# Optimization experiments

Measured on AMD Instinct MI355X. Metric: run time of the kernel, lower is better.

## Reference

```python
import jax, jax.numpy as jnp
import numpy as np

EPS = 1e-8       # module eps
LN_EPS = 1e-5    # torch LayerNorm default
TEMP = 1.0       # relevance_temperature
STRENGTH = 1.0   # reweight_strength default (None -> 1.0)

Q, W, A = 64, 16, 64
D, C, H = 512, 512, 512


def _ln(x, g, b):
    m = x.mean(-1, keepdims=True)
    v = ((x - m) ** 2).mean(-1, keepdims=True)
    return (x - m) / jnp.sqrt(v + LN_EPS) * g + b


def _mlp(x, g, b, w1, b1, w2, b2):
    # LayerNorm -> Linear -> GELU(exact) -> Linear
    h = jax.nn.gelu(_ln(x, g, b) @ w1 + b1, approximate=False)
    return h @ w2 + b2


def setup_inputs() -> dict:
    key = jax.random.key(0)
    ks = iter(jax.random.split(key, 40))
    s = 0.02

    def lin(din, dout):
        return (jax.random.normal(next(ks), (din, dout), jnp.float32) * s,
                jnp.zeros((dout,), jnp.float32))

    inp = {
        "query_atoms": jax.random.normal(next(ks), (Q, A, D), jnp.float32),
        "query_masses": jax.random.uniform(next(ks), (Q, A), jnp.float32, 0.01, 1.0),
        "class_atoms": jax.random.normal(next(ks), (W, A, D), jnp.float32),
        "class_masses": jax.random.uniform(next(ks), (W, A), jnp.float32, 0.01, 1.0),
        "class_summary": jax.random.normal(next(ks), (W, C), jnp.float32),
        "episode_context": jax.random.normal(next(ks), (W, C), jnp.float32),
    }
    # query_proj
    inp["qg"], inp["qb"] = jnp.ones((D,), jnp.float32), jnp.zeros((D,), jnp.float32)
    inp["qw1"], inp["qb1"] = lin(D, H)
    inp["qw2"], inp["qb2"] = lin(H, H)
    # atom_proj
    inp["ag"], inp["ab"] = jnp.ones((D,), jnp.float32), jnp.zeros((D,), jnp.float32)
    inp["aw1"], inp["ab1"] = lin(D, H)
    inp["aw2"], inp["ab2"] = lin(H, H)
    # context_proj (input 2*C)
    inp["cg"], inp["cb"] = jnp.ones((2 * C,), jnp.float32), jnp.zeros((2 * C,), jnp.float32)
    inp["cw1"], inp["cb1"] = lin(2 * C, H)
    inp["cw2"], inp["cb2"] = lin(H, H)
    # relevance_head (input 4*H, output 1)
    inp["rg"], inp["rb"] = jnp.ones((4 * H,), jnp.float32), jnp.zeros((4 * H,), jnp.float32)
    inp["rw1"], inp["rb1"] = lin(4 * H, H)
    inp["rw2"], inp["rb2"] = lin(H, 1)
    return inp


def reference(query_atoms, query_masses, class_atoms, class_masses,
              class_summary, episode_context,
              qg, qb, qw1, qb1, qw2, qb2,
              ag, ab, aw1, ab1, aw2, ab2,
              cg, cb, cw1, cb1, cw2, cb2,
              rg, rb, rw1, rb1, rw2, rb2):
    # normalize query masses, pool query atoms -> [Q, D]
    qm = jnp.maximum(query_masses, 0.0)
    qm = qm / jnp.maximum(qm.sum(-1, keepdims=True), EPS)
    pooled = jnp.einsum('qa,qad->qd', qm, query_atoms)

    qh = _mlp(pooled, qg, qb, qw1, qb1, qw2, qb2)            # [Q, H]
    ah = _mlp(class_atoms, ag, ab, aw1, ab1, aw2, ab2)       # [W, A, H]
    ch = _mlp(jnp.concatenate([class_summary, episode_context], -1),
              cg, cb, cw1, cb1, cw2, cb2)                    # [W, H]

    nq, (way, na, h) = qh.shape[0], ah.shape
    a4 = jnp.broadcast_to(ah[None], (nq, way, na, h))
    q4 = jnp.broadcast_to(qh[:, None, None, :], (nq, way, na, h))
    c4 = jnp.broadcast_to(ch[None, :, None, :], (nq, way, na, h))
    fused = jnp.concatenate([a4, q4, a4 * q4, jnp.abs(a4 - q4) + c4], -1)  # [Q,W,A,4H]

    relevance = _mlp(fused, rg, rb, rw1, rb1, rw2, rb2)[..., 0]  # [Q, W, A]

    combined = jnp.log(jnp.maximum(class_masses, EPS))[None] + relevance / TEMP
    rew = jax.nn.softmax(combined, axis=-1)
    mixed = (1.0 - STRENGTH) * class_masses[None] + STRENGTH * rew
    mixed = mixed / jnp.maximum(mixed.sum(-1, keepdims=True), EPS)
    entropy = -(mixed * jnp.log(jnp.maximum(mixed, EPS))).sum(-1)  # [Q, W]
    return mixed, entropy
```

## Files before the change

kernel.cpp:

```cpp
#include <hip/hip_runtime.h>


#define DEV static __device__ __forceinline__

typedef __attribute__((ext_vector_type(8))) __bf16 bf16x8;
typedef __attribute__((ext_vector_type(4))) float f32x4;
typedef unsigned short ushort_t;

DEV ushort_t f2bf(float f) {
  unsigned u = __builtin_bit_cast(unsigned, f);
  u = (u + 0x7fffu + ((u >> 16) & 1u)) >> 16;
  return (ushort_t)u;
}

DEV float gelu_fast(float x) {
  const float y = x * 0.70710678118654752f;
  const float z = fabsf(y);
  const float t = __fdividef(1.0f, 1.0f + 0.3275911f * z);
  float p = 1.061405429f;
  p = p * t - 1.453152027f;
  p = p * t + 1.421413741f;
  p = p * t - 0.284496736f;
  p = p * t + 0.254829592f;
  const float e = 1.0f - p * t * __expf(-z * z);
  const float erfv = copysignf(e, y);
  return 0.5f * x * (1.0f + erfv);
}

DEV float gelu_sig(float x) {
  return x * __frcp_rn(1.0f + __expf(-1.702f * x));
}

#define OFF_XQB    0
#define OFF_XAB    16384
#define OFF_XCB    278528
#define OFF_HAB    286720
#define OFF_HQB    548864
#define OFF_HCB    565248
#define OFF_AHB    569344
#define OFF_QH     1093632
#define OFF_S1     1126400
#define OFF_B1     1126912
#define OFF_WT2    1127424
#define OFF_RW1LOT 1389568
#define OFF_RW1MIT 1520640
#define OFF_AW1T   1651712
#define OFF_QW1T   1782784
#define OFF_CW1T   1913856
#define OFF_AW2T   2176000
#define OFF_QW2T   2307072
#define OFF_CW2T   2438144
#define OFF_YA     OFF_AW1T
#define OFF_YQ     OFF_AW2T
#define OFF_CHH    OFF_XCB
#define OFF_AHHS   OFF_XAB
#define OFF_QHS    OFF_XQB


DEV void transpose_tile(const float* __restrict__ src, int koff, int kt, int ct,
                        ushort_t* __restrict__ dst, int ldk, float* sh, int tid) {
  float (*t)[65] = (float(*)[65])sh;
  for (int idx = tid; idx < 4096; idx += 512) {
    const int r = idx >> 6, c = idx & 63;
    t[r][c] = src[(koff + kt + r) * 512 + ct + c];
  }
  __syncthreads();
  for (int idx = tid; idx < 4096; idx += 512) {
    const int c = idx >> 6, r = idx & 63;
    dst[(ct + c) * ldk + kt + r] = f2bf(t[r][c]);
  }
}

__global__ __launch_bounds__(512) void pre0_kernel(
    const float* __restrict__ qa, const float* __restrict__ qm,
    const float* __restrict__ ca, const float* __restrict__ csum,
    const float* __restrict__ ectx,
    const float* __restrict__ qg, const float* __restrict__ qb,
    const float* __restrict__ ag, const float* __restrict__ ab,
    const float* __restrict__ cg, const float* __restrict__ cb,
    const float* __restrict__ rw1, const float* __restrict__ rg,
    const float* __restrict__ rb,
    const float* __restrict__ aw1, const float* __restrict__ qw1,
    const float* __restrict__ cw1, const float* __restrict__ aw2,
    const float* __restrict__ qw2, const float* __restrict__ cw2,
    float* __restrict__ ws) {
  __shared__ float sh[4160];
  const int b = blockIdx.x, tid = threadIdx.x, l = tid & 63, wv = tid >> 6;

  if (b < 128) {
    ushort_t* WT = (ushort_t*)(ws + OFF_WT2);
    float (*t)[65] = (float(*)[65])sh;
    const int kt = (b >> 3) << 6;
    const int ct = (b & 7) << 6;
    for (int idx = tid; idx < 4096; idx += 512) {
      const int r = idx >> 6, c = idx & 63;
      t[r][c] = rg[1024 + kt + r] * rw1[(1024 + kt + r) * 512 + ct + c];
    }
    __syncthreads();
    for (int idx = tid; idx < 4096; idx += 512) {
      const int c = idx >> 6, r = idx & 63;
      const int n = ct + c, k2 = kt + r;
      WT[((k2 >> 5) << 14) + (n << 5) + (k2 & 31)] = f2bf(t[r][c]);
    }
  } else if (b < 192) {
    const int bb = b - 128;
    transpose_tile(rw1, 0, (bb >> 3) << 6, (bb & 7) << 6,
                   (ushort_t*)(ws + OFF_RW1LOT), 512, sh, tid);
  } else if (b < 256) {
    const int bb = b - 192;
    transpose_tile(rw1, 512, (bb >> 3) << 6, (bb & 7) << 6,
                   (ushort_t*)(ws + OFF_RW1MIT), 512, sh, tid);
  } else if (b < 320) {
    const int bb = b - 256;
    transpose_tile(aw1, 0, (bb >> 3) << 6, (bb & 7) << 6,
                   (ushort_t*)(ws + OFF_AW1T), 512, sh, tid);
  } else if (b < 384) {
    const int bb = b - 320;
    transpose_tile(qw1, 0, (bb >> 3) << 6, (bb & 7) << 6,
                   (ushort_t*)(ws + OFF_QW1T), 512, sh, tid);
  } else if (b < 512) {
    const int bb = b - 384;
    transpose_tile(cw1, 0, (bb >> 3) << 6, (bb & 7) << 6,
                   (ushort_t*)(ws + OFF_CW1T), 1024, sh, tid);
  } else if (b < 576) {
    const int bb = b - 512;
    transpose_tile(aw2, 0, (bb >> 3) << 6, (bb & 7) << 6,
                   (ushort_t*)(ws + OFF_AW2T), 512, sh, tid);
  } else if (b < 640) {
    const int bb = b - 576;
    transpose_tile(qw2, 0, (bb >> 3) << 6, (bb & 7) << 6,
                   (ushort_t*)(ws + OFF_QW2T), 512, sh, tid);
  } else if (b < 704) {
    const int bb = b - 640;
    transpose_tile(cw2, 0, (bb >> 3) << 6, (bb & 7) << 6,
                   (ushort_t*)(ws + OFF_CW2T), 512, sh, tid);
  } else if (b < 720) {
    const int kc = (b - 704) << 7;
    float s0 = 0.f, s1 = 0.f, b0 = 0.f, b1v = 0.f;
    for (int k = kc; k < kc + 128; k += 2) {
      const float wa = rw1[(k << 9) + tid];
      const float wb = rw1[((k + 1) << 9) + tid];
      s0 += rg[k] * wa; b0 += rb[k] * wa;
      s1 += rg[k + 1] * wb; b1v += rb[k + 1] * wb;
    }
    atomicAdd(ws + OFF_S1 + tid, s0 + s1);
    atomicAdd(ws + OFF_B1 + tid, b0 + b1v);
  } else if (b < 784) {
    const int q = b - 720;
    if (wv == 0) {
      float m = fmaxf(qm[(q << 6) + l], 0.f);
      sh[l] = m;
      float s = m;
#pragma unroll
      for (int off = 1; off < 64; off <<= 1) s += __shfl_xor(s, off);
      if (l == 0) sh[64] = 1.0f / fmaxf(s, 1e-8f);
    }
    __syncthreads();
    const float sinv = sh[64];
    const float* qaq = qa + (q << 15) + tid;
    float v0 = 0.f, v1 = 0.f, v2 = 0.f, v3 = 0.f;
#pragma unroll 4
    for (int a = 0; a < 64; a += 4) {
      v0 += sh[a] * qaq[a << 9];
      v1 += sh[a + 1] * qaq[(a + 1) << 9];
      v2 += sh[a + 2] * qaq[(a + 2) << 9];
      v3 += sh[a + 3] * qaq[(a + 3) << 9];
    }
    const float v = (v0 + v1 + v2 + v3) * sinv;
    float s = v, ss = v * v;
#pragma unroll
    for (int off = 1; off < 64; off <<= 1) {
      s += __shfl_xor(s, off); ss += __shfl_xor(ss, off);
    }
    if (l == 0) { sh[128 + wv] = s; sh[136 + wv] = ss; }
    __syncthreads();
    float st = 0.f, sst = 0.f;
#pragma unroll
    for (int i = 0; i < 8; ++i) { st += sh[128 + i]; sst += sh[136 + i]; }
    const float mu = st * (1.0f / 512.0f);
    const float rstd = rsqrtf(sst * (1.0f / 512.0f) - mu * mu + 1e-5f);
    ((ushort_t*)(ws + OFF_XQB))[(q << 9) + tid] =
        f2bf((v - mu) * rstd * qg[tid] + qb[tid]);
  } else if (b < 912) {
    const int row = ((b - 784) << 3) + wv;
    const float* crow = ca + (row << 9);
    float x[8];
    float s = 0.f, ss = 0.f;
#pragma unroll
    for (int i = 0; i < 8; ++i) {
      x[i] = crow[l + (i << 6)];
      s += x[i]; ss += x[i] * x[i];
    }
#pragma unroll
    for (int off = 1; off < 64; off <<= 1) {
      s += __shfl_xor(s, off); ss += __shfl_xor(ss, off);
    }
    const float mu = s * (1.0f / 512.0f);
    const float rstd = rsqrtf(ss * (1.0f / 512.0f) - mu * mu + 1e-5f);
    ushort_t* xab = (ushort_t*)(ws + OFF_XAB);
#pragma unroll
    for (int i = 0; i < 8; ++i) {
      const int k = l + (i << 6);
      xab[(row << 9) + k] = f2bf((x[i] - mu) * rstd * ag[k] + ab[k]);
    }
  } else {
    const int w = b - 912;
    const float v0 = csum[(w << 9) + tid];
    const float v1 = ectx[(w << 9) + tid];
    float s = v0 + v1, ss = v0 * v0 + v1 * v1;
#pragma unroll
    for (int off = 1; off < 64; off <<= 1) {
      s += __shfl_xor(s, off); ss += __shfl_xor(ss, off);
    }
    if (l == 0) { sh[wv] = s; sh[8 + wv] = ss; }
    __syncthreads();
    float st = 0.f, sst = 0.f;
#pragma unroll
    for (int i = 0; i < 8; ++i) { st += sh[i]; sst += sh[8 + i]; }
    const float mu = st * (1.0f / 1024.0f);
    const float rstd = rsqrtf(sst * (1.0f / 1024.0f) - mu * mu + 1e-5f);
    ushort_t* xcb = (ushort_t*)(ws + OFF_XCB);
    xcb[(w << 10) + tid] = f2bf((v0 - mu) * rstd * cg[tid] + cb[tid]);
    xcb[(w << 10) + 512 + tid] =
        f2bf((v1 - mu) * rstd * cg[512 + tid] + cb[512 + tid]);
  }
}

template <int PHASE>
__global__ __launch_bounds__(256) void gemm_kernel(
    float* __restrict__ ws, const float* __restrict__ ba,
    const float* __restrict__ bq, const float* __restrict__ bc,
    const float* __restrict__ rg) {
  const int b = blockIdx.x, tid = threadIdx.x;
  const int l = tid & 63, wv = tid >> 6;

  const ushort_t* A; const ushort_t* BT;
  float* outF = nullptr; ushort_t* outB = nullptr; ushort_t* outS = nullptr;
  ushort_t* outU = nullptr;
  const float* bias = nullptr; const float* scl = nullptr;
  int K, t;

  if (PHASE == 1) {
    if (b < 512) {
      A = (const ushort_t*)(ws + OFF_XAB); BT = (const ushort_t*)(ws + OFF_AW1T);
      K = 512; outB = (ushort_t*)(ws + OFF_HAB); bias = ba;
      t = (b << 2) + wv;
    } else if (b < 544) {
      A = (const ushort_t*)(ws + OFF_XQB); BT = (const ushort_t*)(ws + OFF_QW1T);
      K = 512; outB = (ushort_t*)(ws + OFF_HQB); bias = bq;
      t = ((b - 512) << 2) + wv;
    } else {
      A = (const ushort_t*)(ws + OFF_XCB); BT = (const ushort_t*)(ws + OFF_CW1T);
      K = 1024; outB = (ushort_t*)(ws + OFF_HCB); bias = bc;
      t = ((b - 544) << 2) + wv;
    }
  } else if (PHASE == 2) {
    if (b < 512) {
      A = (const ushort_t*)(ws + OFF_HAB); BT = (const ushort_t*)(ws + OFF_AW2T);
      K = 512; outU = (ushort_t*)(ws + OFF_AHB);
      outS = (ushort_t*)(ws + OFF_AHHS); bias = ba; scl = rg;
      t = (b << 2) + wv;
    } else if (b < 544) {
      A = (const ushort_t*)(ws + OFF_HQB); BT = (const ushort_t*)(ws + OFF_QW2T);
      K = 512; outF = ws + OFF_QH;
      outS = (ushort_t*)(ws + OFF_QHS); bias = bq; scl = rg + 512;
      t = ((b - 512) << 2) + wv;
    } else {
      A = (const ushort_t*)(ws + OFF_HCB); BT = (const ushort_t*)(ws + OFF_CW2T);
      K = 512; outF = ws + OFF_CHH; bias = bc;
      t = ((b - 544) << 2) + wv;
    }
  } else {
    if (b < 512) {
      A = (const ushort_t*)(ws + OFF_AHHS); BT = (const ushort_t*)(ws + OFF_RW1LOT);
      K = 512; outF = ws + OFF_YA;
      t = (b << 2) + wv;
    } else {
      A = (const ushort_t*)(ws + OFF_QHS); BT = (const ushort_t*)(ws + OFF_RW1MIT);
      K = 512; outF = ws + OFF_YQ;
      t = ((b - 512) << 2) + wv;
    }
  }

  const int rt = t >> 5, ct = t & 31;
  const int r0 = rt << 4, c0 = ct << 4;
  const int kh = (l >> 4) << 3;
  const ushort_t* ap = A + (r0 + (l & 15)) * K + kh;
  const ushort_t* bp = BT + (c0 + (l & 15)) * K + kh;

  f32x4 acc = {};
  const int nst = K >> 5;
#pragma unroll 8
  for (int ks = 0; ks < nst; ++ks) {
    const bf16x8 afr = __builtin_bit_cast(bf16x8, *(const uint4*)(ap + (ks << 5)));
    const bf16x8 bfr = __builtin_bit_cast(bf16x8, *(const uint4*)(bp + (ks << 5)));
    acc = __builtin_amdgcn_mfma_f32_16x16x32_bf16(afr, bfr, acc, 0, 0, 0);
  }

  const int rsub = (l >> 4) << 2, col = c0 + (l & 15);
#pragma unroll
  for (int j = 0; j < 4; ++j) {
    const int row = r0 + rsub + j;
    float v = acc[j];
    if (PHASE == 1) {
      outB[(row << 9) + col] = f2bf(gelu_fast(v + bias[col]));
    } else if (PHASE == 2) {
      v += bias[col];
      if (outU) outU[(row << 9) + col] = f2bf(v);
      if (outF) outF[(row << 9) + col] = v;
      if (outS) outS[(row << 9) + col] = f2bf(v * scl[col]);
    } else {
      outF[(row << 9) + col] = v;
    }
  }
}

__global__ __launch_bounds__(512, 2) void main_kernel(
    const ushort_t* __restrict__ AHB, const float* __restrict__ QH,
    const float* __restrict__ CH, const ushort_t* __restrict__ WT2,
    const float* __restrict__ Ya, const float* __restrict__ Yq,
    const float* __restrict__ S1, const float* __restrict__ B1,
    const float* __restrict__ rb1, const float* __restrict__ rw2,
    const float* __restrict__ rb2, const float* __restrict__ cmass,
    float* __restrict__ out) {
  extern __shared__ char smem_raw[];
  float* qs = (float*)smem_raw;
  float* cs = qs + 1024;
  float* s1_s = cs + 512;
  float* s2_s = s1_s + 128;
  float* rel_s = s2_s + 128;
  float* misc = rel_s + 128;
  uint4* ab4 = (uint4*)(smem_raw + 8192);
  uint4* apv = (uint4*)(smem_raw + 8192 + 65536);

  const int tid = threadIdx.x;
  const int l = tid & 63;
  const int wv = tid >> 6;
  const int w = blockIdx.x & 15;
  const int q0 = (blockIdx.x >> 4) << 1;

  {
    const uint4* src = (const uint4*)(AHB + ((w << 6) << 9));
#pragma unroll
    for (int i = 0; i < 16; ++i) {
      const int u = tid + (i << 9);
      const int row = u >> 7, c16 = u & 127;
      ab4[(row << 7) + (c16 ^ (row & 7))] = src[u];
    }
  }
  qs[tid] = QH[(q0 << 9) + tid];
  qs[tid + 512] = QH[(q0 << 9) + 512 + tid];
  cs[tid] = CH[(w << 9) + tid];
  if (tid < 128) { s1_s[tid] = 0.f; s2_s[tid] = 0.f; rel_s[tid] = 0.f; }
  __syncthreads();

  const int p = wv >> 2;
  const int s = wv & 3;
  const int rloc = (s << 4) + (l & 15);
  const float* qsrc = qs + (p << 9);
  const int kh = (l >> 4) << 3;
  const int ar_base = rloc << 7;
  const int rsw = rloc & 7;
  float s1a = 0.f, s2a = 0.f;

#define BUILD(C, B) do { \
    _Pragma("unroll") for (int ksl_ = 0; ksl_ < 4; ++ksl_) { \
      const int kg_ = ((C) << 7) + (ksl_ << 5) + kh; \
      const int ka_ = kg_ & 511; \
      const bf16x8 av8_ = __builtin_bit_cast(bf16x8, \
          ab4[ar_base + ((ka_ >> 3) ^ rsw)]); \
      union { __bf16 bv[8]; uint4 u4; } pk_; \
      _Pragma("unroll") for (int h_ = 0; h_ < 2; ++h_) { \
        const float4 qv_ = *(const float4*)(qsrc + ka_ + (h_ << 2)); \
        const float a0_ = (float)av8_[(h_ << 2) + 0]; \
        const float a1_ = (float)av8_[(h_ << 2) + 1]; \
        const float a2_ = (float)av8_[(h_ << 2) + 2]; \
        const float a3_ = (float)av8_[(h_ << 2) + 3]; \
        float v0_, v1_, v2_, v3_; \
        if ((C) < 4) { \
          v0_ = a0_ * qv_.x; v1_ = a1_ * qv_.y; \
          v2_ = a2_ * qv_.z; v3_ = a3_ * qv_.w; \
          s1a += (a0_ + a1_ + a2_ + a3_) + (v0_ + v1_ + v2_ + v3_); \
          s2a += (a0_ * a0_ + a1_ * a1_ + a2_ * a2_ + a3_ * a3_) + \
                 (v0_ * v0_ + v1_ * v1_ + v2_ * v2_ + v3_ * v3_); \
        } else { \
          const float4 c_ = *(const float4*)(cs + ka_ + (h_ << 2)); \
          v0_ = fabsf(a0_ - qv_.x) + c_.x; \
          v1_ = fabsf(a1_ - qv_.y) + c_.y; \
          v2_ = fabsf(a2_ - qv_.z) + c_.z; \
          v3_ = fabsf(a3_ - qv_.w) + c_.w; \
          s1a += v0_ + v1_ + v2_ + v3_; \
          s2a += v0_ * v0_ + v1_ * v1_ + v2_ * v2_ + v3_ * v3_; \
        } \
        pk_.bv[(h_ << 2) + 0] = (__bf16)v0_; \
        pk_.bv[(h_ << 2) + 1] = (__bf16)v1_; \
        pk_.bv[(h_ << 2) + 2] = (__bf16)v2_; \
        pk_.bv[(h_ << 2) + 3] = (__bf16)v3_; \
      } \
      apv[((B) << 11) + (p << 10) + (ksl_ << 8) + (s << 6) + l] = pk_.u4; \
    } } while (0)

  BUILD(0, 0);
  if ((wv & 3) == 0) {
    float sq = 0.f, sqq = 0.f;
#pragma unroll
    for (int it = 0; it < 8; ++it) {
      const float vq = qsrc[l + (it << 6)];
      sq += vq; sqq += vq * vq;
    }
#pragma unroll
    for (int off = 1; off < 64; off <<= 1) {
      sq += __shfl_xor(sq, off); sqq += __shfl_xor(sqq, off);
    }
    if (l == 0) { misc[(p << 1)] = sq; misc[(p << 1) + 1] = sqq; }
  }
  __syncthreads();

  f32x4 acc0[4][4] = {}, acc1[4][4] = {};
  const int ncb = (wv << 6) + (l & 15);
  const int boff = (ncb << 5) + kh;
#pragma unroll
  for (int c = 0; c < 8; ++c) {
    if (c < 7) {
      BUILD(c + 1, (c + 1) & 1);
    } else {
      s1a += __shfl_xor(s1a, 16); s1a += __shfl_xor(s1a, 32);
      s2a += __shfl_xor(s2a, 16); s2a += __shfl_xor(s2a, 32);
      if ((l >> 4) == 0) {
        atomicAdd(&s1_s[(p << 6) + rloc], s1a);
        atomicAdd(&s2_s[(p << 6) + rloc], s2a);
      }
    }
    const uint4* cbuf = apv + ((c & 1) << 11);
    const ushort_t* wb = WT2 + ((c << 2) << 14) + boff;
    uint4 bn0 = *(const uint4*)(wb);
    uint4 bn1 = *(const uint4*)(wb + (16 << 5));
    uint4 bn2 = *(const uint4*)(wb + (32 << 5));
    uint4 bn3 = *(const uint4*)(wb + (48 << 5));
#pragma unroll
    for (int ksl = 0; ksl < 4; ++ksl) {
      const bf16x8 bf0 = __builtin_bit_cast(bf16x8, bn0);
      const bf16x8 bf1 = __builtin_bit_cast(bf16x8, bn1);
      const bf16x8 bf2 = __builtin_bit_cast(bf16x8, bn2);
      const bf16x8 bf3 = __builtin_bit_cast(bf16x8, bn3);
      if (ksl < 3) {
        const ushort_t* wn = wb + ((ksl + 1) << 14);
        bn0 = *(const uint4*)(wn);
        bn1 = *(const uint4*)(wn + (16 << 5));
        bn2 = *(const uint4*)(wn + (32 << 5));
        bn3 = *(const uint4*)(wn + (48 << 5));
      }
      bf16x8 afr;
      __builtin_amdgcn_s_setprio(1);
#pragma unroll
      for (int fr = 0; fr < 4; ++fr) {
        afr = __builtin_bit_cast(bf16x8, cbuf[(ksl << 8) + (fr << 6) + l]);
        acc0[fr][0] = __builtin_amdgcn_mfma_f32_16x16x32_bf16(afr, bf0, acc0[fr][0], 0, 0, 0);
        acc0[fr][1] = __builtin_amdgcn_mfma_f32_16x16x32_bf16(afr, bf1, acc0[fr][1], 0, 0, 0);
        acc0[fr][2] = __builtin_amdgcn_mfma_f32_16x16x32_bf16(afr, bf2, acc0[fr][2], 0, 0, 0);
        acc0[fr][3] = __builtin_amdgcn_mfma_f32_16x16x32_bf16(afr, bf3, acc0[fr][3], 0, 0, 0);
      }
#pragma unroll
      for (int fr = 0; fr < 4; ++fr) {
        afr = __builtin_bit_cast(bf16x8, cbuf[(1 << 10) + (ksl << 8) + (fr << 6) + l]);
        acc1[fr][0] = __builtin_amdgcn_mfma_f32_16x16x32_bf16(afr, bf0, acc1[fr][0], 0, 0, 0);
        acc1[fr][1] = __builtin_amdgcn_mfma_f32_16x16x32_bf16(afr, bf1, acc1[fr][1], 0, 0, 0);
        acc1[fr][2] = __builtin_amdgcn_mfma_f32_16x16x32_bf16(afr, bf2, acc1[fr][2], 0, 0, 0);
        acc1[fr][3] = __builtin_amdgcn_mfma_f32_16x16x32_bf16(afr, bf3, acc1[fr][3], 0, 0, 0);
      }
      __builtin_amdgcn_s_setprio(0);
    }
    __syncthreads();
  }
#undef BUILD

  if (tid < 128) {
    const int pp = tid >> 6;
    const float s1r = s1_s[tid] + misc[pp << 1];
    const float s2r = s2_s[tid] + misc[(pp << 1) + 1];
    const float mu = s1r * (1.0f / 2048.0f);
    const float rs = rsqrtf(s2r * (1.0f / 2048.0f) - mu * mu + 1e-5f);
    s1_s[tid] = mu;
    s2_s[tid] = rs;
  }
  __syncthreads();

  {
    float yqv0[4], yqv1[4], s1c[4], b1c[4], w2c[4];
#pragma unroll
    for (int cf = 0; cf < 4; ++cf) {
      const int n = ncb + (cf << 4);
      yqv0[cf] = Yq[(q0 << 9) + n];
      yqv1[cf] = Yq[((q0 + 1) << 9) + n];
      s1c[cf] = S1[n];
      b1c[cf] = B1[n] + rb1[n];
      w2c[cf] = rw2[n];
    }
    const float* yab = Ya + (w << 15) + ncb;
    const int rsub = (l >> 4) << 2;
#pragma unroll
    for (int fr = 0; fr < 4; ++fr) {
#pragma unroll
      for (int j = 0; j < 4; ++j) {
        const int r = (fr << 4) + rsub + j;
        const float mu0 = s1_s[r], rs0 = s2_s[r];
        const float mu1 = s1_s[64 + r], rs1 = s2_s[64 + r];
        float rp0 = 0.f, rp1 = 0.f;
#pragma unroll
        for (int cf = 0; cf < 4; ++cf) {
          const float ya = yab[(r << 9) + (cf << 4)];
          const float c0v = ya + yqv0[cf] - mu0 * s1c[cf];
          const float c1v = ya + yqv1[cf] - mu1 * s1c[cf];
          rp0 += gelu_sig(fmaf(rs0, acc0[fr][cf][j] + c0v, b1c[cf])) * w2c[cf];
          rp1 += gelu_sig(fmaf(rs1, acc1[fr][cf][j] + c1v, b1c[cf])) * w2c[cf];
        }
        rp0 += __shfl_xor(rp0, 1); rp0 += __shfl_xor(rp0, 2);
        rp0 += __shfl_xor(rp0, 4); rp0 += __shfl_xor(rp0, 8);
        rp1 += __shfl_xor(rp1, 1); rp1 += __shfl_xor(rp1, 2);
        rp1 += __shfl_xor(rp1, 4); rp1 += __shfl_xor(rp1, 8);
        if ((l & 15) == 0) {
          atomicAdd(&rel_s[r], rp0);
          atomicAdd(&rel_s[64 + r], rp1);
        }
      }
    }
  }
  __syncthreads();

  if (tid < 128) {
    const int pp = tid >> 6, a = tid & 63;
    const int qw = ((q0 + pp) << 4) + w;
    const float relv = rel_s[(pp << 6) + a] + rb2[0];
    const float x = logf(fmaxf(cmass[(w << 6) + a], 1e-8f)) + relv;
    float m = x;
#pragma unroll
    for (int off = 1; off < 64; off <<= 1) m = fmaxf(m, __shfl_xor(m, off));
    const float pv = expf(x - m);
    float sv = pv;
#pragma unroll
    for (int off = 1; off < 64; off <<= 1) sv += __shfl_xor(sv, off);
    float mix = pv / fmaxf(sv, 1e-8f);
    float s2 = mix;
#pragma unroll
    for (int off = 1; off < 64; off <<= 1) s2 += __shfl_xor(s2, off);
    mix = mix / fmaxf(s2, 1e-8f);
    const float et = -mix * logf(fmaxf(mix, 1e-8f));
    float ent = et;
#pragma unroll
    for (int off = 1; off < 64; off <<= 1) ent += __shfl_xor(ent, off);
    out[(qw << 6) + a] = mix;
    if (a == 0) out[65536 + qw] = ent;
  }
}

extern "C" void kernel_launch(void* const* d_in, const int* in_sizes, int n_in,
                              void* d_out, int out_size, void* d_ws, size_t ws_size,
                              hipStream_t stream) {
  (void)in_sizes; (void)n_in; (void)out_size; (void)ws_size;
  const float* q_atoms = (const float*)d_in[0];
  const float* q_mass  = (const float*)d_in[1];
  const float* c_atoms = (const float*)d_in[2];
  const float* c_mass  = (const float*)d_in[3];
  const float* c_sum   = (const float*)d_in[4];
  const float* e_ctx   = (const float*)d_in[5];
  const float* qg  = (const float*)d_in[6];  const float* qb  = (const float*)d_in[7];
  const float* qw1 = (const float*)d_in[8];  const float* qb1 = (const float*)d_in[9];
  const float* qw2 = (const float*)d_in[10]; const float* qb2 = (const float*)d_in[11];
  const float* ag  = (const float*)d_in[12]; const float* ab  = (const float*)d_in[13];
  const float* aw1 = (const float*)d_in[14]; const float* ab1 = (const float*)d_in[15];
  const float* aw2 = (const float*)d_in[16]; const float* ab2 = (const float*)d_in[17];
  const float* cg  = (const float*)d_in[18]; const float* cb  = (const float*)d_in[19];
  const float* cw1 = (const float*)d_in[20]; const float* cb1 = (const float*)d_in[21];
  const float* cw2 = (const float*)d_in[22]; const float* cb2 = (const float*)d_in[23];
  const float* rg  = (const float*)d_in[24]; const float* rb  = (const float*)d_in[25];
  const float* rw1 = (const float*)d_in[26]; const float* rb1 = (const float*)d_in[27];
  const float* rw2 = (const float*)d_in[28]; const float* rb2 = (const float*)d_in[29];

  float* ws = (float*)d_ws;
  float* out = (float*)d_out;

  hipMemsetAsync(ws + OFF_S1, 0, 1024 * sizeof(float), stream);
  pre0_kernel<<<928, 512, 0, stream>>>(q_atoms, q_mass, c_atoms, c_sum, e_ctx,
                                       qg, qb, ag, ab, cg, cb, rw1, rg, rb,
                                       aw1, qw1, cw1, aw2, qw2, cw2, ws);
  gemm_kernel<1><<<552, 256, 0, stream>>>(ws, ab1, qb1, cb1, rg);
  gemm_kernel<2><<<552, 256, 0, stream>>>(ws, ab2, qb2, cb2, rg);
  gemm_kernel<3><<<544, 256, 0, stream>>>(ws, nullptr, nullptr, nullptr, rg);

  static const size_t MAIN_SMEM = 8192 + 65536 + 65536;
  hipFuncSetAttribute((const void*)main_kernel,
                      hipFuncAttributeMaxDynamicSharedMemorySize, (int)MAIN_SMEM);
  main_kernel<<<512, 512, MAIN_SMEM, stream>>>(
      (const ushort_t*)(ws + OFF_AHB), ws + OFF_QH, ws + OFF_CHH,
      (const ushort_t*)(ws + OFF_WT2), ws + OFF_YA, ws + OFF_YQ,
      ws + OFF_S1, ws + OFF_B1, rb1, rw2, rb2, c_mass, out);
}
```

Measured before the change: 151.4 us.

## Split main kernel over atom halves and move softmax into separate kernel

Each main_kernel block now handles 32 of the 64 atoms for a (query-pair, way) instead of all 64. This halves shared memory and accumulator registers, doubles the grid to 1024 blocks and raises the occupancy hint to 4 blocks per CU. Because the per-way softmax over 64 atoms then spans two blocks, relevance logits are written to workspace and a new softmax_kernel computes the mixed weights and entropy. The cost is an extra launch and global round trip, and each block still streams the full second-layer weight matrix, so total weight traffic doubles.

```diff
diff --git a/kernel.cpp b/kernel.cpp
--- a/kernel.cpp
+++ b/kernel.cpp
@@ -55,6 +55,7 @@
 #define OFF_CHH    OFF_XCB
 #define OFF_AHHS   OFF_XAB
 #define OFF_QHS    OFF_XQB
+#define OFF_REL    OFF_XAB
 
 
 DEV void transpose_tile(const float* __restrict__ src, int koff, int kt, int ct,
@@ -315,60 +316,58 @@
   }
 }
 
-__global__ __launch_bounds__(512, 2) void main_kernel(
+__global__ __launch_bounds__(512, 4) void main_kernel(
     const ushort_t* __restrict__ AHB, const float* __restrict__ QH,
     const float* __restrict__ CH, const ushort_t* __restrict__ WT2,
     const float* __restrict__ Ya, const float* __restrict__ Yq,
     const float* __restrict__ S1, const float* __restrict__ B1,
     const float* __restrict__ rb1, const float* __restrict__ rw2,
-    const float* __restrict__ rb2, const float* __restrict__ cmass,
-    float* __restrict__ out) {
+    const float* __restrict__ rb2, float* __restrict__ rel) {
   extern __shared__ char smem_raw[];
   float* qs = (float*)smem_raw;
   float* cs = qs + 1024;
   float* s1_s = cs + 512;
-  float* s2_s = s1_s + 128;
-  float* rel_s = s2_s + 128;
-  float* misc = rel_s + 128;
+  float* s2_s = s1_s + 64;
+  float* rel_s = s2_s + 64;
+  float* misc = rel_s + 64;
   uint4* ab4 = (uint4*)(smem_raw + 8192);
-  uint4* apv = (uint4*)(smem_raw + 8192 + 65536);
+  uint4* apv = (uint4*)(smem_raw + 8192 + 32768);
 
   const int tid = threadIdx.x;
   const int l = tid & 63;
   const int wv = tid >> 6;
-  const int w = blockIdx.x & 15;
-  const int q0 = (blockIdx.x >> 4) << 1;
+  const int h = blockIdx.x & 1;
+  const int w = (blockIdx.x >> 1) & 15;
+  const int q0 = (blockIdx.x >> 5) << 1;
 
   {
-    const uint4* src = (const uint4*)(AHB + ((w << 6) << 9));
-#pragma unroll
-    for (int i = 0; i < 16; ++i) {
+    const uint4* src = (const uint4*)(AHB + (((w << 6) + (h << 5)) << 9));
+#pragma unroll
+    for (int i = 0; i < 4; ++i) {
       const int u = tid + (i << 9);
-      const int row = u >> 7, c16 = u & 127;
-      ab4[(row << 7) + (c16 ^ (row & 7))] = src[u];
+      const int row = u >> 6, c16 = u & 63;
+      ab4[(row << 6) + (c16 ^ (row & 7))] = src[u];
     }
   }
   qs[tid] = QH[(q0 << 9) + tid];
   qs[tid + 512] = QH[(q0 << 9) + 512 + tid];
   cs[tid] = CH[(w << 9) + tid];
-  if (tid < 128) { s1_s[tid] = 0.f; s2_s[tid] = 0.f; rel_s[tid] = 0.f; }
+  if (tid < 64) { s1_s[tid] = 0.f; s2_s[tid] = 0.f; rel_s[tid] = 0.f; }
   __syncthreads();
 
   const int p = wv >> 2;
   const int s = wv & 3;
-  const int rloc = (s << 4) + (l & 15);
   const float* qsrc = qs + (p << 9);
   const int kh = (l >> 4) << 3;
-  const int ar_base = rloc << 7;
-  const int rsw = rloc & 7;
-  float s1a = 0.f, s2a = 0.f;
+  float s1a[2] = {0.f, 0.f}, s2a[2] = {0.f, 0.f};
 
 #define BUILD(C, B) do { \
-    _Pragma("unroll") for (int ksl_ = 0; ksl_ < 4; ++ksl_) { \
-      const int kg_ = ((C) << 7) + (ksl_ << 5) + kh; \
+    _Pragma("unroll") for (int fr_ = 0; fr_ < 2; ++fr_) { \
+      const int row_ = (fr_ << 4) + (l & 15); \
+      const int kg_ = ((C) << 7) + (s << 5) + kh; \
       const int ka_ = kg_ & 511; \
       const bf16x8 av8_ = __builtin_bit_cast(bf16x8, \
-          ab4[ar_base + ((ka_ >> 3) ^ rsw)]); \
+          ab4[(row_ << 6) + ((ka_ >> 3) ^ (row_ & 7))]); \
       union { __bf16 bv[8]; uint4 u4; } pk_; \
       _Pragma("unroll") for (int h_ = 0; h_ < 2; ++h_) { \
         const float4 qv_ = *(const float4*)(qsrc + ka_ + (h_ << 2)); \
@@ -380,8 +379,8 @@
         if ((C) < 4) { \
           v0_ = a0_ * qv_.x; v1_ = a1_ * qv_.y; \
           v2_ = a2_ * qv_.z; v3_ = a3_ * qv_.w; \
-          s1a += (a0_ + a1_ + a2_ + a3_) + (v0_ + v1_ + v2_ + v3_); \
-          s2a += (a0_ * a0_ + a1_ * a1_ + a2_ * a2_ + a3_ * a3_) + \
+          s1a[fr_] += (a0_ + a1_ + a2_ + a3_) + (v0_ + v1_ + v2_ + v3_); \
+          s2a[fr_] += (a0_ * a0_ + a1_ * a1_ + a2_ * a2_ + a3_ * a3_) + \
                  (v0_ * v0_ + v1_ * v1_ + v2_ * v2_ + v3_ * v3_); \
         } else { \
           const float4 c_ = *(const float4*)(cs + ka_ + (h_ << 2)); \
@@ -389,15 +388,15 @@
           v1_ = fabsf(a1_ - qv_.y) + c_.y; \
           v2_ = fabsf(a2_ - qv_.z) + c_.z; \
           v3_ = fabsf(a3_ - qv_.w) + c_.w; \
-          s1a += v0_ + v1_ + v2_ + v3_; \
-          s2a += v0_ * v0_ + v1_ * v1_ + v2_ * v2_ + v3_ * v3_; \
+          s1a[fr_] += v0_ + v1_ + v2_ + v3_; \
+          s2a[fr_] += v0_ * v0_ + v1_ * v1_ + v2_ * v2_ + v3_ * v3_; \
         } \
         pk_.bv[(h_ << 2) + 0] = (__bf16)v0_; \
         pk_.bv[(h_ << 2) + 1] = (__bf16)v1_; \
         pk_.bv[(h_ << 2) + 2] = (__bf16)v2_; \
         pk_.bv[(h_ << 2) + 3] = (__bf16)v3_; \
       } \
-      apv[((B) << 11) + (p << 10) + (ksl_ << 8) + (s << 6) + l] = pk_.u4; \
+      apv[((B) << 10) + (p << 9) + (s << 7) + (fr_ << 6) + l] = pk_.u4; \
     } } while (0)
 
   BUILD(0, 0);
@@ -416,7 +415,7 @@
   }
   __syncthreads();
 
-  f32x4 acc0[4][4] = {}, acc1[4][4] = {};
+  f32x4 acc0[2][4] = {}, acc1[2][4] = {};
   const int ncb = (wv << 6) + (l & 15);
   const int boff = (ncb << 5) + kh;
 #pragma unroll
@@ -424,14 +423,18 @@
     if (c < 7) {
       BUILD(c + 1, (c + 1) & 1);
     } else {
-      s1a += __shfl_xor(s1a, 16); s1a += __shfl_xor(s1a, 32);
-      s2a += __shfl_xor(s2a, 16); s2a += __shfl_xor(s2a, 32);
-      if ((l >> 4) == 0) {
-        atomicAdd(&s1_s[(p << 6) + rloc], s1a);
-        atomicAdd(&s2_s[(p << 6) + rloc], s2a);
+#pragma unroll
+      for (int fr = 0; fr < 2; ++fr) {
+        float s1v = s1a[fr], s2v = s2a[fr];
+        s1v += __shfl_xor(s1v, 16); s1v += __shfl_xor(s1v, 32);
+        s2v += __shfl_xor(s2v, 16); s2v += __shfl_xor(s2v, 32);
+        if ((l >> 4) == 0) {
+          atomicAdd(&s1_s[(p << 5) + (fr << 4) + l], s1v);
+          atomicAdd(&s2_s[(p << 5) + (fr << 4) + l], s2v);
+        }
       }
     }
-    const uint4* cbuf = apv + ((c & 1) << 11);
+    const uint4* cbuf = apv + ((c & 1) << 10);
     const ushort_t* wb = WT2 + ((c << 2) << 14) + boff;
     uint4 bn0 = *(const uint4*)(wb);
     uint4 bn1 = *(const uint4*)(wb + (16 << 5));
@@ -453,16 +456,16 @@
       bf16x8 afr;
       __builtin_amdgcn_s_setprio(1);
 #pragma unroll
-      for (int fr = 0; fr < 4; ++fr) {
-        afr = __builtin_bit_cast(bf16x8, cbuf[(ksl << 8) + (fr << 6) + l]);
+      for (int fr = 0; fr < 2; ++fr) {
+        afr = __builtin_bit_cast(bf16x8, cbuf[(ksl << 7) + (fr << 6) + l]);
         acc0[fr][0] = __builtin_amdgcn_mfma_f32_16x16x32_bf16(afr, bf0, acc0[fr][0], 0, 0, 0);
         acc0[fr][1] = __builtin_amdgcn_mfma_f32_16x16x32_bf16(afr, bf1, acc0[fr][1], 0, 0, 0);
         acc0[fr][2] = __builtin_amdgcn_mfma_f32_16x16x32_bf16(afr, bf2, acc0[fr][2], 0, 0, 0);
         acc0[fr][3] = __builtin_amdgcn_mfma_f32_16x16x32_bf16(afr, bf3, acc0[fr][3], 0, 0, 0);
       }
 #pragma unroll
-      for (int fr = 0; fr < 4; ++fr) {
-        afr = __builtin_bit_cast(bf16x8, cbuf[(1 << 10) + (ksl << 8) + (fr << 6) + l]);
+      for (int fr = 0; fr < 2; ++fr) {
+        afr = __builtin_bit_cast(bf16x8, cbuf[(1 << 9) + (ksl << 7) + (fr << 6) + l]);
         acc1[fr][0] = __builtin_amdgcn_mfma_f32_16x16x32_bf16(afr, bf0, acc1[fr][0], 0, 0, 0);
         acc1[fr][1] = __builtin_amdgcn_mfma_f32_16x16x32_bf16(afr, bf1, acc1[fr][1], 0, 0, 0);
         acc1[fr][2] = __builtin_amdgcn_mfma_f32_16x16x32_bf16(afr, bf2, acc1[fr][2], 0, 0, 0);
@@ -474,8 +477,8 @@
   }
 #undef BUILD
 
-  if (tid < 128) {
-    const int pp = tid >> 6;
+  if (tid < 64) {
+    const int pp = tid >> 5;
     const float s1r = s1_s[tid] + misc[pp << 1];
     const float s2r = s2_s[tid] + misc[(pp << 1) + 1];
     const float mu = s1r * (1.0f / 2048.0f);
@@ -496,15 +499,15 @@
       b1c[cf] = B1[n] + rb1[n];
       w2c[cf] = rw2[n];
     }
-    const float* yab = Ya + (w << 15) + ncb;
+    const float* yab = Ya + (w << 15) + ((h << 5) << 9) + ncb;
     const int rsub = (l >> 4) << 2;
 #pragma unroll
-    for (int fr = 0; fr < 4; ++fr) {
+    for (int fr = 0; fr < 2; ++fr) {
 #pragma unroll
       for (int j = 0; j < 4; ++j) {
         const int r = (fr << 4) + rsub + j;
         const float mu0 = s1_s[r], rs0 = s2_s[r];
-        const float mu1 = s1_s[64 + r], rs1 = s2_s[64 + r];
+        const float mu1 = s1_s[32 + r], rs1 = s2_s[32 + r];
         float rp0 = 0.f, rp1 = 0.f;
 #pragma unroll
         for (int cf = 0; cf < 4; ++cf) {
@@ -520,37 +523,45 @@
         rp1 += __shfl_xor(rp1, 4); rp1 += __shfl_xor(rp1, 8);
         if ((l & 15) == 0) {
           atomicAdd(&rel_s[r], rp0);
-          atomicAdd(&rel_s[64 + r], rp1);
+          atomicAdd(&rel_s[32 + r], rp1);
         }
       }
     }
   }
   __syncthreads();
 
-  if (tid < 128) {
-    const int pp = tid >> 6, a = tid & 63;
-    const int qw = ((q0 + pp) << 4) + w;
-    const float relv = rel_s[(pp << 6) + a] + rb2[0];
-    const float x = logf(fmaxf(cmass[(w << 6) + a], 1e-8f)) + relv;
-    float m = x;
-#pragma unroll
-    for (int off = 1; off < 64; off <<= 1) m = fmaxf(m, __shfl_xor(m, off));
-    const float pv = expf(x - m);
-    float sv = pv;
-#pragma unroll
-    for (int off = 1; off < 64; off <<= 1) sv += __shfl_xor(sv, off);
-    float mix = pv / fmaxf(sv, 1e-8f);
-    float s2 = mix;
-#pragma unroll
-    for (int off = 1; off < 64; off <<= 1) s2 += __shfl_xor(s2, off);
-    mix = mix / fmaxf(s2, 1e-8f);
-    const float et = -mix * logf(fmaxf(mix, 1e-8f));
-    float ent = et;
-#pragma unroll
-    for (int off = 1; off < 64; off <<= 1) ent += __shfl_xor(ent, off);
-    out[(qw << 6) + a] = mix;
-    if (a == 0) out[65536 + qw] = ent;
-  }
+  if (tid < 64) {
+    const int pp = tid >> 5, rr = tid & 31;
+    rel[((q0 + pp) << 10) + (w << 6) + (h << 5) + rr] = rel_s[tid];
+  }
+}
+
+__global__ __launch_bounds__(1024) void softmax_kernel(
+    const float* __restrict__ rel, const float* __restrict__ cmass,
+    const float* __restrict__ rb2, float* __restrict__ out) {
+  const int tid = threadIdx.x, l = tid & 63, wv = tid >> 6;
+  const int g = (blockIdx.x << 4) + wv;
+  const int q = g >> 4, w = g & 15;
+  const float relv = rel[(q << 10) + (w << 6) + l] + rb2[0];
+  const float x = logf(fmaxf(cmass[(w << 6) + l], 1e-8f)) + relv;
+  float m = x;
+#pragma unroll
+  for (int off = 1; off < 64; off <<= 1) m = fmaxf(m, __shfl_xor(m, off));
+  const float pv = expf(x - m);
+  float sv = pv;
+#pragma unroll
+  for (int off = 1; off < 64; off <<= 1) sv += __shfl_xor(sv, off);
+  float mix = pv / fmaxf(sv, 1e-8f);
+  float s2 = mix;
+#pragma unroll
+  for (int off = 1; off < 64; off <<= 1) s2 += __shfl_xor(s2, off);
+  mix = mix / fmaxf(s2, 1e-8f);
+  const float et = -mix * logf(fmaxf(mix, 1e-8f));
+  float ent = et;
+#pragma unroll
+  for (int off = 1; off < 64; off <<= 1) ent += __shfl_xor(ent, off);
+  out[(g << 6) + l] = mix;
+  if (l == 0) out[65536 + g] = ent;
 }
 
 extern "C" void kernel_launch(void* const* d_in, const int* in_sizes, int n_in,
@@ -587,11 +598,12 @@
   gemm_kernel<2><<<552, 256, 0, stream>>>(ws, ab2, qb2, cb2, rg);
   gemm_kernel<3><<<544, 256, 0, stream>>>(ws, nullptr, nullptr, nullptr, rg);
 
-  static const size_t MAIN_SMEM = 8192 + 65536 + 65536;
+  static const size_t MAIN_SMEM = 8192 + 32768 + 32768;
   hipFuncSetAttribute((const void*)main_kernel,
                       hipFuncAttributeMaxDynamicSharedMemorySize, (int)MAIN_SMEM);
-  main_kernel<<<512, 512, MAIN_SMEM, stream>>>(
+  main_kernel<<<1024, 512, MAIN_SMEM, stream>>>(
       (const ushort_t*)(ws + OFF_AHB), ws + OFF_QH, ws + OFF_CHH,
       (const ushort_t*)(ws + OFF_WT2), ws + OFF_YA, ws + OFF_YQ,
-      ws + OFF_S1, ws + OFF_B1, rb1, rw2, rb2, c_mass, out);
-}
+      ws + OFF_S1, ws + OFF_B1, rb1, rw2, rb2, ws + OFF_REL);
+  softmax_kernel<<<64, 1024, 0, stream>>>(ws + OFF_REL, c_mass, rb2, out);
+}
```

Result: slower. 187.9 us (+24.1%).
